# Kernel optimization log

Measured on AMD Instinct MI355X. Metric: run time of the kernel, lower is better.

The kernel has to match this reference:

```python
import jax, jax.numpy as jnp
import numpy as np

B, C = 2, 4
SPATIAL = (128, 128, 128)
N_PTS = 32          # num_points_per_class
THR = 0.5           # threshold


def setup_inputs() -> dict:
    key = jax.random.key(0)
    logits = jax.random.normal(key, (B, C) + SPATIAL, dtype=jnp.float32)
    return {"logits": logits}


def _extract_points(logits):
    """Vectorized equivalent of the per-(batch,class) nonzero/topk loop.

    For every (b, c): softmax prob > THR defines candidates; top-k by prob
    selects up to N_PTS points. Classes are visited in the original order
    (foreground 1..C-1, then background 0); valid points are compacted to
    the front per batch element; padding has label -1 and coords 0.
    Output width is fixed at C*N_PTS (jit-friendly) instead of the batch
    max count, but all valid (coord, label) entries and their order match.
    """
    b, c = logits.shape[:2]
    spatial = logits.shape[2:]
    dims = len(spatial)
    S = int(np.prod(spatial))
    probs = jax.nn.softmax(logits, axis=1).reshape(b, c, S)  # [b,c,S]
    # class visitation order: 1..C-1 then 0 (background last)
    order = jnp.concatenate([jnp.arange(1, c), jnp.arange(1)])  # [c]
    probs = probs[:, order]                                    # [b,c,S]
    score = jnp.where(probs > THR, probs, -jnp.inf)
    top_vals, top_idx = jax.lax.top_k(score, N_PTS)            # [b,c,N_PTS]
    valid = top_vals > -jnp.inf                                # [b,c,N_PTS]
    coords = jnp.stack(jnp.unravel_index(top_idx, spatial), axis=-1)  # [b,c,N_PTS,dims]
    labels = jnp.where(valid, order[None, :, None], -1)        # [b,c,N_PTS]
    coords = jnp.where(valid[..., None], coords, 0)
    # flatten classes and compact valid points to the front (stable sort)
    N = c * N_PTS
    labels = labels.reshape(b, N)
    coords = coords.reshape(b, N, dims)
    perm = jnp.argsort((labels < 0).astype(jnp.int32), axis=1, stable=True)  # [b,N]
    labels = jnp.take_along_axis(labels, perm, axis=1)
    coords = jnp.take_along_axis(coords, perm[..., None], axis=1)
    return coords.astype(jnp.int32), labels.astype(jnp.int32)


def reference(logits):
    coords, labels = _extract_points(logits)
    return coords, labels
```

## Files before the change

### kernel.cpp

```cpp
#include <hip/hip_runtime.h>
#include <stdint.h>

#define Bn 2
#define Cn 4
#define Sn (128 * 128 * 128)
#define NPTS 32
#define NBINS 1025
#define THRf 0.5f
#define PB 4096
#define BT 512
#define FCAP 2048

__device__ __forceinline__ int bin_of_bits(unsigned int u) {
    return (int)((u - 0x3F000000u) >> 13);
}

__device__ __forceinline__ void softmax_argmax4(float l0, float l1, float l2, float l3,
                                                int* cm_out, float* p_out) {
    float m = fmaxf(fmaxf(l0, l1), fmaxf(l2, l3));
    float e0 = expf(l0 - m);
    float e1 = expf(l1 - m);
    float e2 = expf(l2 - m);
    float e3 = expf(l3 - m);
    float s = ((e0 + e1) + e2) + e3;
    float em = e0; int cm = 0;
    if (e1 > em) { em = e1; cm = 1; }
    if (e2 > em) { em = e2; cm = 2; }
    if (e3 > em) { em = e3; cm = 3; }
    *cm_out = cm;
    *p_out = em / s;
}

__global__ __launch_bounds__(BT) void fused_kernel(const float* __restrict__ logits,
                                                   unsigned int* __restrict__ cnt,
                                                   uint2* __restrict__ cand,
                                                   int cap) {
    __shared__ unsigned int lh[Cn * NBINS];
    __shared__ unsigned int lcut[Cn], cls_cnt[Cn], cls_base[Cn], cls_pos[Cn];
    const int b = blockIdx.y;
    const int t = threadIdx.x;
    const int lane = t & 63;
    for (int j = t; j < Cn * NBINS; j += BT) lh[j] = 0u;
    if (t < Cn) { lcut[t] = 0u; cls_cnt[t] = 0u; cls_pos[t] = 0u; }
    __syncthreads();

    const float* base = logits + (size_t)b * Cn * Sn;
    const float4* s0 = (const float4*)base;
    const float4* s1 = (const float4*)(base + Sn);
    const float4* s2 = (const float4*)(base + 2 * Sn);
    const float4* s3 = (const float4*)(base + 3 * Sn);
    const int qs = blockIdx.x * (PB / 4);
    unsigned int pk[PB / BT];
    #pragma unroll
    for (int it = 0; it < PB / 4 / BT; ++it) {
        int q = qs + it * BT + t;
        float4 v0 = s0[q], v1 = s1[q], v2 = s2[q], v3 = s3[q];
        const float* a0 = &v0.x; const float* a1 = &v1.x;
        const float* a2 = &v2.x; const float* a3 = &v3.x;
        #pragma unroll
        for (int k = 0; k < 4; ++k) {
            int cm; float p;
            softmax_argmax4(a0[k], a1[k], a2[k], a3[k], &cm, &p);
            unsigned int pv = 0u;
            if (p > THRf) {
                unsigned int off = __float_as_uint(p) - 0x3F000000u;
                atomicAdd(&lh[cm * NBINS + (int)(off >> 13)], 1u);
                pv = (off << 2) | (unsigned int)cm;
            }
            pk[it * 4 + k] = pv;
        }
    }
    __syncthreads();

    {
        const int wave = t >> 6;
        if (wave < Cn) {
            const unsigned int* h = &lh[wave * NBINS];
            const int lo = lane * 17;
            unsigned int cs = 0;
            #pragma unroll
            for (int k = 0; k < 17; ++k) {
                int bin = lo + k;
                if (bin < NBINS) cs += h[bin];
            }
            unsigned int S = cs;
            #pragma unroll
            for (int off = 1; off < 64; off <<= 1) {
                unsigned int v = __shfl_down(S, off, 64);
                if (lane + off < 64) S += v;
            }
            unsigned int suf = S - cs;
            if (S >= NPTS && suf < NPTS) {
                unsigned int acc = suf;
                int hi = min(lo + 16, NBINS - 1);
                for (int bin = hi; bin >= lo; --bin) {
                    acc += h[bin];
                    if (acc >= NPTS) {
                        lcut[wave] = (unsigned int)bin;
                        cls_cnt[wave] = acc;
                        break;
                    }
                }
            }
            if (lane == 0 && S < NPTS) cls_cnt[wave] = S;
        }
    }
    __syncthreads();

    if (t < Cn && cls_cnt[t] > 0)
        cls_base[t] = atomicAdd(&cnt[b * Cn + t], cls_cnt[t]);
    __syncthreads();

    #pragma unroll
    for (int j = 0; j < PB / BT; ++j) {
        unsigned int pv = pk[j];
        if (pv != 0u) {
            unsigned int cm = pv & 3u;
            if ((pv >> 15) >= lcut[cm]) {
                unsigned int pos = cls_base[cm] + atomicAdd(&cls_pos[cm], 1u);
                if (pos < (unsigned int)cap) {
                    int it = j >> 2, k = j & 3;
                    unsigned int idx = (unsigned int)((qs + it * BT + t) * 4 + k);
                    cand[(size_t)(b * Cn + cm) * cap + pos] =
                        make_uint2(0x3F000000u + (pv >> 2), idx);
                }
            }
        }
    }
}

__global__ __launch_bounds__(1024) void select_emit(const unsigned int* __restrict__ cnt,
                                                    const uint2* __restrict__ cand,
                                                    int cap,
                                                    unsigned int* __restrict__ validn,
                                                    uint2* __restrict__ topk,
                                                    unsigned int* __restrict__ done,
                                                    int* __restrict__ out) {
    __shared__ unsigned int lh[NBINS];
    __shared__ uint2 fbuf[FCAP];
    __shared__ unsigned int s_m, s_T, s_old;
    const int bc = blockIdx.x, t = threadIdx.x;
    const int b = bc >> 2;
    const int n = min((int)cnt[bc], cap);
    for (int j = t; j < NBINS; j += 1024) lh[j] = 0u;
    if (t == 0) { s_m = 0u; s_T = 0u; }
    __syncthreads();
    const uint2* src = cand + (size_t)bc * cap;
    for (int j = t; j < n; j += 1024)
        atomicAdd(&lh[bin_of_bits(src[j].x)], 1u);
    __syncthreads();
    if (t < 64) {
        const int lane = t;
        const int lo = lane * 17;
        unsigned int cs = 0;
        #pragma unroll
        for (int k = 0; k < 17; ++k) {
            int bin = lo + k;
            if (bin < NBINS) cs += lh[bin];
        }
        unsigned int S = cs;
        #pragma unroll
        for (int off = 1; off < 64; off <<= 1) {
            unsigned int v = __shfl_down(S, off, 64);
            if (lane + off < 64) S += v;
        }
        unsigned int suf = S - cs;
        if (S >= NPTS && suf < NPTS) {
            unsigned int acc = suf;
            int hi = min(lo + 16, NBINS - 1);
            for (int bin = hi; bin >= lo; --bin) {
                acc += lh[bin];
                if (acc >= NPTS) { s_T = (unsigned int)bin; break; }
            }
        }
    }
    __syncthreads();
    const unsigned int T = s_T;
    for (int j = t; j < n; j += 1024) {
        uint2 e = src[j];
        if ((unsigned int)bin_of_bits(e.x) >= T) {
            unsigned int pos = atomicAdd(&s_m, 1u);
            if (pos < FCAP) fbuf[pos] = e;
        }
    }
    __syncthreads();
    const int m = min((int)s_m, FCAP);
    const int vn = min(n, NPTS);
    if (t == 0) validn[bc] = (unsigned int)vn;
    for (int i = t; i < m; i += 1024) {
        uint2 e = fbuf[i];
        int rank = 0;
        for (int j = 0; j < m; ++j) {
            uint2 o = fbuf[j];
            rank += (int)((o.x > e.x) || (o.x == e.x && o.y < e.y));
        }
        if (rank < vn) topk[bc * NPTS + rank] = e;
    }

    __threadfence();
    __syncthreads();
    if (t == 0) s_old = atomicAdd(&done[b], 1u);
    __syncthreads();
    if (s_old == 3u) {
        __threadfence();
        __shared__ int pre[Cn + 1];
        if (t == 0) {
            int acc = 0;
            for (int oc = 0; oc < Cn; ++oc) {
                pre[oc] = acc;
                acc += (int)validn[b * Cn + ((oc + 1) & 3)];
            }
            pre[Cn] = acc;
        }
        __syncthreads();
        if (t < Cn * NPTS) {
            const int j = t;
            int label = -1, z = 0, y = 0, x = 0;
            if (j < pre[Cn]) {
                int oc = 0;
                while (j >= pre[oc + 1]) ++oc;
                int c = (oc + 1) & 3;
                int r = j - pre[oc];
                uint2 e = topk[(b * Cn + c) * NPTS + r];
                int idx = (int)e.y;
                z = idx >> 14;
                y = (idx >> 7) & 127;
                x = idx & 127;
                label = c;
            }
            int* coords = out;
            int* labels = out + Bn * Cn * NPTS * 3;
            int bo = b * Cn * NPTS + j;
            coords[bo * 3 + 0] = z;
            coords[bo * 3 + 1] = y;
            coords[bo * 3 + 2] = x;
            labels[bo] = label;
        }
    }
}

extern "C" void kernel_launch(void* const* d_in, const int* in_sizes, int n_in,
                              void* d_out, int out_size, void* d_ws, size_t ws_size,
                              hipStream_t stream) {
    const float* logits = (const float*)d_in[0];
    int* out = (int*)d_out;

    unsigned int* cnt = (unsigned int*)d_ws;
    unsigned int* done = cnt + Bn * Cn;
    unsigned int* validn = done + Bn;
    uint2* topk = (uint2*)(validn + Bn * Cn);
    uint2* cand = topk + Bn * Cn * NPTS;
    size_t fixed = (size_t)((char*)cand - (char*)d_ws);
    int cap = (int)((ws_size - fixed) / (Bn * Cn * sizeof(uint2)));
    if (cap > (1 << 18)) cap = 1 << 18;
    if (cap < 4096) cap = 4096;

    hipMemsetAsync(cnt, 0, (Bn * Cn + Bn) * sizeof(unsigned int), stream);

    dim3 grid(Sn / PB, Bn);
    fused_kernel<<<grid, BT, 0, stream>>>(logits, cnt, cand, cap);
    select_emit<<<Bn * Cn, 1024, 0, stream>>>(cnt, cand, cap, validn, topk, done, out);
}
```

Baseline: 120.0 us.

## Fuse top-k selection and emission into last-finishing block of main kernel

After: 345.2 us. 2.88x slower.

```diff
diff --git a/kernel.cpp b/kernel.cpp
--- a/kernel.cpp
+++ b/kernel.cpp
@@ -9,7 +9,7 @@
 #define THRf 0.5f
 #define PB 4096
 #define BT 512
-#define FCAP 2048
+#define FB 512
 
 __device__ __forceinline__ int bin_of_bits(unsigned int u) {
     return (int)((u - 0x3F000000u) >> 13);
@@ -34,9 +34,18 @@
 __global__ __launch_bounds__(BT) void fused_kernel(const float* __restrict__ logits,
                                                    unsigned int* __restrict__ cnt,
                                                    uint2* __restrict__ cand,
-                                                   int cap) {
+                                                   int cap,
+                                                   unsigned int* __restrict__ done,
+                                                   int* __restrict__ out) {
     __shared__ unsigned int lh[Cn * NBINS];
     __shared__ unsigned int lcut[Cn], cls_cnt[Cn], cls_base[Cn], cls_pos[Cn];
+    __shared__ unsigned int s_old;
+    __shared__ uint2 fbuf[Cn * FB];
+    __shared__ uint2 stopk[Cn * NPTS];
+    __shared__ int s_n[Cn];
+    __shared__ unsigned int s_T[Cn], s_m[Cn];
+    __shared__ int pre[Cn + 1];
+
     const int b = blockIdx.y;
     const int t = threadIdx.x;
     const int lane = t & 63;
@@ -127,115 +136,119 @@
             }
         }
     }
-}
-
-__global__ __launch_bounds__(1024) void select_emit(const unsigned int* __restrict__ cnt,
-                                                    const uint2* __restrict__ cand,
-                                                    int cap,
-                                                    unsigned int* __restrict__ validn,
-                                                    uint2* __restrict__ topk,
-                                                    unsigned int* __restrict__ done,
-                                                    int* __restrict__ out) {
-    __shared__ unsigned int lh[NBINS];
-    __shared__ uint2 fbuf[FCAP];
-    __shared__ unsigned int s_m, s_T, s_old;
-    const int bc = blockIdx.x, t = threadIdx.x;
-    const int b = bc >> 2;
-    const int n = min((int)cnt[bc], cap);
-    for (int j = t; j < NBINS; j += 1024) lh[j] = 0u;
-    if (t == 0) { s_m = 0u; s_T = 0u; }
-    __syncthreads();
-    const uint2* src = cand + (size_t)bc * cap;
-    for (int j = t; j < n; j += 1024)
-        atomicAdd(&lh[bin_of_bits(src[j].x)], 1u);
-    __syncthreads();
-    if (t < 64) {
-        const int lane = t;
-        const int lo = lane * 17;
-        unsigned int cs = 0;
-        #pragma unroll
-        for (int k = 0; k < 17; ++k) {
-            int bin = lo + k;
-            if (bin < NBINS) cs += lh[bin];
-        }
-        unsigned int S = cs;
-        #pragma unroll
-        for (int off = 1; off < 64; off <<= 1) {
-            unsigned int v = __shfl_down(S, off, 64);
-            if (lane + off < 64) S += v;
-        }
-        unsigned int suf = S - cs;
-        if (S >= NPTS && suf < NPTS) {
-            unsigned int acc = suf;
-            int hi = min(lo + 16, NBINS - 1);
-            for (int bin = hi; bin >= lo; --bin) {
-                acc += lh[bin];
-                if (acc >= NPTS) { s_T = (unsigned int)bin; break; }
-            }
-        }
-    }
-    __syncthreads();
-    const unsigned int T = s_T;
-    for (int j = t; j < n; j += 1024) {
-        uint2 e = src[j];
-        if ((unsigned int)bin_of_bits(e.x) >= T) {
-            unsigned int pos = atomicAdd(&s_m, 1u);
-            if (pos < FCAP) fbuf[pos] = e;
-        }
-    }
-    __syncthreads();
-    const int m = min((int)s_m, FCAP);
-    const int vn = min(n, NPTS);
-    if (t == 0) validn[bc] = (unsigned int)vn;
-    for (int i = t; i < m; i += 1024) {
-        uint2 e = fbuf[i];
-        int rank = 0;
-        for (int j = 0; j < m; ++j) {
-            uint2 o = fbuf[j];
-            rank += (int)((o.x > e.x) || (o.x == e.x && o.y < e.y));
-        }
-        if (rank < vn) topk[bc * NPTS + rank] = e;
-    }
 
     __threadfence();
     __syncthreads();
     if (t == 0) s_old = atomicAdd(&done[b], 1u);
     __syncthreads();
-    if (s_old == 3u) {
-        __threadfence();
-        __shared__ int pre[Cn + 1];
-        if (t == 0) {
-            int acc = 0;
-            for (int oc = 0; oc < Cn; ++oc) {
-                pre[oc] = acc;
-                acc += (int)validn[b * Cn + ((oc + 1) & 3)];
-            }
-            pre[Cn] = acc;
-        }
-        __syncthreads();
-        if (t < Cn * NPTS) {
-            const int j = t;
-            int label = -1, z = 0, y = 0, x = 0;
-            if (j < pre[Cn]) {
-                int oc = 0;
-                while (j >= pre[oc + 1]) ++oc;
-                int c = (oc + 1) & 3;
-                int r = j - pre[oc];
-                uint2 e = topk[(b * Cn + c) * NPTS + r];
-                int idx = (int)e.y;
-                z = idx >> 14;
-                y = (idx >> 7) & 127;
-                x = idx & 127;
-                label = c;
-            }
-            int* coords = out;
-            int* labels = out + Bn * Cn * NPTS * 3;
-            int bo = b * Cn * NPTS + j;
-            coords[bo * 3 + 0] = z;
-            coords[bo * 3 + 1] = y;
-            coords[bo * 3 + 2] = x;
-            labels[bo] = label;
-        }
+    if (s_old != (unsigned int)(gridDim.x - 1)) return;
+    __threadfence();
+
+    for (int j = t; j < Cn * NBINS; j += BT) lh[j] = 0u;
+    if (t < Cn) {
+        s_n[t] = min((int)cnt[b * Cn + t], cap);
+        s_T[t] = 0u;
+        s_m[t] = 0u;
+    }
+    __syncthreads();
+
+    for (int c = 0; c < Cn; ++c) {
+        const uint2* src = cand + (size_t)(b * Cn + c) * cap;
+        const int n = s_n[c];
+        for (int j = t; j < n; j += BT)
+            atomicAdd(&lh[c * NBINS + bin_of_bits(src[j].x)], 1u);
+    }
+    __syncthreads();
+
+    {
+        const int wave = t >> 6;
+        if (wave < Cn) {
+            const unsigned int* h = &lh[wave * NBINS];
+            const int lo = lane * 17;
+            unsigned int cs = 0;
+            #pragma unroll
+            for (int k = 0; k < 17; ++k) {
+                int bin = lo + k;
+                if (bin < NBINS) cs += h[bin];
+            }
+            unsigned int S = cs;
+            #pragma unroll
+            for (int off = 1; off < 64; off <<= 1) {
+                unsigned int v = __shfl_down(S, off, 64);
+                if (lane + off < 64) S += v;
+            }
+            unsigned int suf = S - cs;
+            if (S >= NPTS && suf < NPTS) {
+                unsigned int acc = suf;
+                int hi = min(lo + 16, NBINS - 1);
+                for (int bin = hi; bin >= lo; --bin) {
+                    acc += h[bin];
+                    if (acc >= NPTS) { s_T[wave] = (unsigned int)bin; break; }
+                }
+            }
+        }
+    }
+    __syncthreads();
+
+    for (int c = 0; c < Cn; ++c) {
+        const uint2* src = cand + (size_t)(b * Cn + c) * cap;
+        const int n = s_n[c];
+        const unsigned int T = s_T[c];
+        for (int j = t; j < n; j += BT) {
+            uint2 e = src[j];
+            if ((unsigned int)bin_of_bits(e.x) >= T) {
+                unsigned int pos = atomicAdd(&s_m[c], 1u);
+                if (pos < FB) fbuf[c * FB + pos] = e;
+            }
+        }
+    }
+    __syncthreads();
+
+    for (int c = 0; c < Cn; ++c) {
+        const int m = min((int)s_m[c], FB);
+        const int vn = min(s_n[c], NPTS);
+        for (int i = t; i < m; i += BT) {
+            uint2 e = fbuf[c * FB + i];
+            int rank = 0;
+            for (int j = 0; j < m; ++j) {
+                uint2 o = fbuf[c * FB + j];
+                rank += (int)((o.x > e.x) || (o.x == e.x && o.y < e.y));
+            }
+            if (rank < vn) stopk[c * NPTS + rank] = e;
+        }
+    }
+    if (t == 0) {
+        int acc = 0;
+        for (int oc = 0; oc < Cn; ++oc) {
+            pre[oc] = acc;
+            acc += min(s_n[(oc + 1) & 3], NPTS);
+        }
+        pre[Cn] = acc;
+    }
+    __syncthreads();
+
+    if (t < Cn * NPTS) {
+        const int j = t;
+        int label = -1, z = 0, y = 0, x = 0;
+        if (j < pre[Cn]) {
+            int oc = 0;
+            while (j >= pre[oc + 1]) ++oc;
+            int c = (oc + 1) & 3;
+            int r = j - pre[oc];
+            uint2 e = stopk[c * NPTS + r];
+            int idx = (int)e.y;
+            z = idx >> 14;
+            y = (idx >> 7) & 127;
+            x = idx & 127;
+            label = c;
+        }
+        int* coords = out;
+        int* labels = out + Bn * Cn * NPTS * 3;
+        int bo = b * Cn * NPTS + j;
+        coords[bo * 3 + 0] = z;
+        coords[bo * 3 + 1] = y;
+        coords[bo * 3 + 2] = x;
+        labels[bo] = label;
     }
 }
 
@@ -247,9 +260,7 @@
 
     unsigned int* cnt = (unsigned int*)d_ws;
     unsigned int* done = cnt + Bn * Cn;
-    unsigned int* validn = done + Bn;
-    uint2* topk = (uint2*)(validn + Bn * Cn);
-    uint2* cand = topk + Bn * Cn * NPTS;
+    uint2* cand = (uint2*)(done + Bn);
     size_t fixed = (size_t)((char*)cand - (char*)d_ws);
     int cap = (int)((ws_size - fixed) / (Bn * Cn * sizeof(uint2)));
     if (cap > (1 << 18)) cap = 1 << 18;
@@ -258,6 +269,5 @@
     hipMemsetAsync(cnt, 0, (Bn * Cn + Bn) * sizeof(unsigned int), stream);
 
     dim3 grid(Sn / PB, Bn);
-    fused_kernel<<<grid, BT, 0, stream>>>(logits, cnt, cand, cap);
-    select_emit<<<Bn * Cn, 1024, 0, stream>>>(cnt, cand, cap, validn, topk, done, out);
-}
+    fused_kernel<<<grid, BT, 0, stream>>>(logits, cnt, cand, cap, done, out);
+}
```

## Fuse select/emit into main kernel via last-block grid sync and global histograms

Applied to the files above, without the earlier changes.

Measured after the change: 128.2 us. 1.07x slower.

```diff
diff --git a/kernel.cpp b/kernel.cpp
--- a/kernel.cpp
+++ b/kernel.cpp
@@ -9,7 +9,7 @@
 #define THRf 0.5f
 #define PB 4096
 #define BT 512
-#define FCAP 2048
+#define FB 1024
 
 __device__ __forceinline__ int bin_of_bits(unsigned int u) {
     return (int)((u - 0x3F000000u) >> 13);
@@ -33,10 +33,21 @@
 
 __global__ __launch_bounds__(BT) void fused_kernel(const float* __restrict__ logits,
                                                    unsigned int* __restrict__ cnt,
+                                                   unsigned int* __restrict__ gh,
                                                    uint2* __restrict__ cand,
-                                                   int cap) {
+                                                   int cap,
+                                                   unsigned int* __restrict__ done,
+                                                   unsigned int* __restrict__ done2,
+                                                   unsigned int* __restrict__ validn,
+                                                   uint2* __restrict__ topk,
+                                                   int* __restrict__ out) {
     __shared__ unsigned int lh[Cn * NBINS];
     __shared__ unsigned int lcut[Cn], cls_cnt[Cn], cls_base[Cn], cls_pos[Cn];
+    __shared__ unsigned int s_old;
+    __shared__ uint2 fbuf[FB];
+    __shared__ unsigned int s_T, s_m;
+    __shared__ int pre[Cn + 1];
+
     const int b = blockIdx.y;
     const int t = threadIdx.x;
     const int lane = t & 63;
@@ -107,6 +118,17 @@
     }
     __syncthreads();
 
+    {
+        const int wave = t >> 6;
+        if (wave < Cn) {
+            const unsigned int* h = &lh[wave * NBINS];
+            unsigned int* g = gh + (size_t)(b * Cn + wave) * NBINS;
+            for (int bin = (int)lcut[wave] + lane; bin < NBINS; bin += 64) {
+                unsigned int v = h[bin];
+                if (v) atomicAdd(&g[bin], v);
+            }
+        }
+    }
     if (t < Cn && cls_cnt[t] > 0)
         cls_base[t] = atomicAdd(&cnt[b * Cn + t], cls_cnt[t]);
     __syncthreads();
@@ -121,36 +143,36 @@
                 if (pos < (unsigned int)cap) {
                     int it = j >> 2, k = j & 3;
                     unsigned int idx = (unsigned int)((qs + it * BT + t) * 4 + k);
-                    cand[(size_t)(b * Cn + cm) * cap + pos] =
-                        make_uint2(0x3F000000u + (pv >> 2), idx);
+                    unsigned long long packed =
+                        ((unsigned long long)idx << 32) | (0x3F000000u + (pv >> 2));
+                    __hip_atomic_store(
+                        (unsigned long long*)&cand[(size_t)(b * Cn + cm) * cap + pos],
+                        packed, __ATOMIC_RELAXED, __HIP_MEMORY_SCOPE_AGENT);
                 }
             }
         }
     }
-}
-
-__global__ __launch_bounds__(1024) void select_emit(const unsigned int* __restrict__ cnt,
-                                                    const uint2* __restrict__ cand,
-                                                    int cap,
-                                                    unsigned int* __restrict__ validn,
-                                                    uint2* __restrict__ topk,
-                                                    unsigned int* __restrict__ done,
-                                                    int* __restrict__ out) {
-    __shared__ unsigned int lh[NBINS];
-    __shared__ uint2 fbuf[FCAP];
-    __shared__ unsigned int s_m, s_T, s_old;
-    const int bc = blockIdx.x, t = threadIdx.x;
-    const int b = bc >> 2;
+
+    __syncthreads();
+    if (t == 0) s_old = atomicAdd(&done[b], 1u);
+    __syncthreads();
+    const unsigned int NX = gridDim.x;
+    if (s_old + 4u < NX) return;
+    const int csel = (int)(NX - 1u - s_old);
+    if (t == 0) {
+        while (__hip_atomic_load(&done[b], __ATOMIC_RELAXED, __HIP_MEMORY_SCOPE_AGENT) < NX)
+            __builtin_amdgcn_s_sleep(2);
+    }
+    __syncthreads();
+    __threadfence();
+
+    const int bc = b * Cn + csel;
+    for (int j = t; j < NBINS; j += BT) lh[j] = gh[(size_t)bc * NBINS + j];
+    if (t == 0) { s_T = 0u; s_m = 0u; }
+    __syncthreads();
     const int n = min((int)cnt[bc], cap);
-    for (int j = t; j < NBINS; j += 1024) lh[j] = 0u;
-    if (t == 0) { s_m = 0u; s_T = 0u; }
-    __syncthreads();
-    const uint2* src = cand + (size_t)bc * cap;
-    for (int j = t; j < n; j += 1024)
-        atomicAdd(&lh[bin_of_bits(src[j].x)], 1u);
-    __syncthreads();
+
     if (t < 64) {
-        const int lane = t;
         const int lo = lane * 17;
         unsigned int cs = 0;
         #pragma unroll
@@ -176,66 +198,85 @@
     }
     __syncthreads();
     const unsigned int T = s_T;
-    for (int j = t; j < n; j += 1024) {
-        uint2 e = src[j];
-        if ((unsigned int)bin_of_bits(e.x) >= T) {
-            unsigned int pos = atomicAdd(&s_m, 1u);
-            if (pos < FCAP) fbuf[pos] = e;
-        }
-    }
-    __syncthreads();
-    const int m = min((int)s_m, FCAP);
+
+    {
+        const uint2* src = cand + (size_t)bc * cap;
+        for (int j0 = t; j0 < n; j0 += BT * 8) {
+            uint2 e[8];
+            #pragma unroll
+            for (int k = 0; k < 8; ++k) {
+                int j = j0 + k * BT;
+                e[k] = src[j < n ? j : (n - 1)];
+            }
+            #pragma unroll
+            for (int k = 0; k < 8; ++k) {
+                int j = j0 + k * BT;
+                if (j < n && (unsigned int)bin_of_bits(e[k].x) >= T) {
+                    unsigned int pos = atomicAdd(&s_m, 1u);
+                    if (pos < FB) fbuf[pos] = e[k];
+                }
+            }
+        }
+    }
+    __syncthreads();
+
+    const int m = min((int)s_m, FB);
     const int vn = min(n, NPTS);
-    if (t == 0) validn[bc] = (unsigned int)vn;
-    for (int i = t; i < m; i += 1024) {
+    if (t == 0)
+        __hip_atomic_store(&validn[bc], (unsigned int)vn,
+                           __ATOMIC_RELAXED, __HIP_MEMORY_SCOPE_AGENT);
+    for (int i = t; i < m; i += BT) {
         uint2 e = fbuf[i];
         int rank = 0;
         for (int j = 0; j < m; ++j) {
             uint2 o = fbuf[j];
             rank += (int)((o.x > e.x) || (o.x == e.x && o.y < e.y));
         }
-        if (rank < vn) topk[bc * NPTS + rank] = e;
-    }
-
+        if (rank < vn) {
+            unsigned long long packed = ((unsigned long long)e.y << 32) | e.x;
+            __hip_atomic_store((unsigned long long*)&topk[bc * NPTS + rank],
+                               packed, __ATOMIC_RELAXED, __HIP_MEMORY_SCOPE_AGENT);
+        }
+    }
+
+    __syncthreads();
+    if (t == 0) s_old = atomicAdd(&done2[b], 1u);
+    __syncthreads();
+    if (s_old != 3u) return;
     __threadfence();
-    __syncthreads();
-    if (t == 0) s_old = atomicAdd(&done[b], 1u);
-    __syncthreads();
-    if (s_old == 3u) {
-        __threadfence();
-        __shared__ int pre[Cn + 1];
-        if (t == 0) {
-            int acc = 0;
-            for (int oc = 0; oc < Cn; ++oc) {
-                pre[oc] = acc;
-                acc += (int)validn[b * Cn + ((oc + 1) & 3)];
-            }
-            pre[Cn] = acc;
-        }
-        __syncthreads();
-        if (t < Cn * NPTS) {
-            const int j = t;
-            int label = -1, z = 0, y = 0, x = 0;
-            if (j < pre[Cn]) {
-                int oc = 0;
-                while (j >= pre[oc + 1]) ++oc;
-                int c = (oc + 1) & 3;
-                int r = j - pre[oc];
-                uint2 e = topk[(b * Cn + c) * NPTS + r];
-                int idx = (int)e.y;
-                z = idx >> 14;
-                y = (idx >> 7) & 127;
-                x = idx & 127;
-                label = c;
-            }
-            int* coords = out;
-            int* labels = out + Bn * Cn * NPTS * 3;
-            int bo = b * Cn * NPTS + j;
-            coords[bo * 3 + 0] = z;
-            coords[bo * 3 + 1] = y;
-            coords[bo * 3 + 2] = x;
-            labels[bo] = label;
-        }
+
+    if (t == 0) {
+        int acc = 0;
+        for (int oc = 0; oc < Cn; ++oc) {
+            pre[oc] = acc;
+            acc += (int)validn[b * Cn + ((oc + 1) & 3)];
+        }
+        pre[Cn] = acc;
+    }
+    __syncthreads();
+
+    if (t < Cn * NPTS) {
+        const int j = t;
+        int label = -1, z = 0, y = 0, x = 0;
+        if (j < pre[Cn]) {
+            int oc = 0;
+            while (j >= pre[oc + 1]) ++oc;
+            int c = (oc + 1) & 3;
+            int r = j - pre[oc];
+            uint2 e = topk[(b * Cn + c) * NPTS + r];
+            int idx = (int)e.y;
+            z = idx >> 14;
+            y = (idx >> 7) & 127;
+            x = idx & 127;
+            label = c;
+        }
+        int* coords = out;
+        int* labels = out + Bn * Cn * NPTS * 3;
+        int bo = b * Cn * NPTS + j;
+        coords[bo * 3 + 0] = z;
+        coords[bo * 3 + 1] = y;
+        coords[bo * 3 + 2] = x;
+        labels[bo] = label;
     }
 }
 
@@ -247,7 +288,9 @@
 
     unsigned int* cnt = (unsigned int*)d_ws;
     unsigned int* done = cnt + Bn * Cn;
-    unsigned int* validn = done + Bn;
+    unsigned int* done2 = done + Bn;
+    unsigned int* gh = done2 + Bn;
+    unsigned int* validn = gh + Bn * Cn * NBINS;
     uint2* topk = (uint2*)(validn + Bn * Cn);
     uint2* cand = topk + Bn * Cn * NPTS;
     size_t fixed = (size_t)((char*)cand - (char*)d_ws);
@@ -255,9 +298,11 @@
     if (cap > (1 << 18)) cap = 1 << 18;
     if (cap < 4096) cap = 4096;
 
-    hipMemsetAsync(cnt, 0, (Bn * Cn + Bn) * sizeof(unsigned int), stream);
+    hipMemsetAsync(cnt, 0,
+                   (size_t)(Bn * Cn + Bn + Bn + Bn * Cn * NBINS) * sizeof(unsigned int),
+                   stream);
 
     dim3 grid(Sn / PB, Bn);
-    fused_kernel<<<grid, BT, 0, stream>>>(logits, cnt, cand, cap);
-    select_emit<<<Bn * Cn, 1024, 0, stream>>>(cnt, cand, cap, validn, topk, done, out);
+    fused_kernel<<<grid, BT, 0, stream>>>(logits, cnt, gh, cand, cap,
+                                          done, done2, validn, topk, out);
 }
```
